# Performance work log

Hardware: AMD Instinct MI355X
Metric: run time of the kernel (lower is better)

Reference implementation:

```python
import jax, jax.numpy as jnp
import numpy as np

N, E, F, NC, G = 50000, 400000, 128, 10, 64
EPS_BN = 1e-5
NEG_SLOPE = 0.2


def gat_conv(x, src, dst, W, a_src, a_dst, b, H, C):
    # PyG GATConv (concat=True): h = xW reshaped [N,H,C]; edge score =
    # leaky_relu(a_src.h_j + a_dst.h_i); softmax over incoming edges of i;
    # out_i = sum_j alpha_ij * h_j, then bias.
    n = x.shape[0]
    h = (x @ W).reshape(n, H, C)
    s_src = jnp.sum(h * a_src, axis=-1)  # [N,H]
    s_dst = jnp.sum(h * a_dst, axis=-1)  # [N,H]
    e = jax.nn.leaky_relu(s_src[src] + s_dst[dst], NEG_SLOPE)  # [E',H]
    m = jax.ops.segment_max(e, dst, num_segments=n)
    e = jnp.exp(e - m[dst])
    z = jax.ops.segment_sum(e, dst, num_segments=n)
    alpha = e / (z[dst] + 1e-16)
    msg = h[src] * alpha[:, :, None]  # [E',H,C]
    out = jax.ops.segment_sum(msg, dst, num_segments=n)
    return out.reshape(n, H * C) + b


def batch_norm(x, g, b):
    mu = jnp.mean(x, axis=0)
    var = jnp.var(x, axis=0)
    return g * (x - mu) * jax.lax.rsqrt(var + EPS_BN) + b


def setup_inputs() -> dict:
    key = jax.random.key(0)
    ks = jax.random.split(key, 32)
    d = {}
    d["x"] = jax.random.normal(ks[0], (N, F), dtype=jnp.float32)
    d["edge_index"] = jax.random.randint(ks[1], (2, E), 0, N, dtype=jnp.int32)
    d["batch"] = jnp.sort(jax.random.randint(ks[2], (N,), 0, G, dtype=jnp.int32))

    def nrm(k, shape, scale=0.1):
        return jax.random.normal(k, shape, dtype=jnp.float32) * scale

    # GATConv1: F -> 16, heads=20
    d["W1"] = nrm(ks[3], (F, 20 * 16))
    d["as1"] = nrm(ks[4], (20, 16))
    d["ad1"] = nrm(ks[5], (20, 16))
    d["b1"] = jnp.zeros((320,), jnp.float32)
    d["g1"], d["be1"] = jnp.ones((320,), jnp.float32), jnp.zeros((320,), jnp.float32)
    d["lw1"], d["lb1"] = nrm(ks[6], (320, 16)), jnp.zeros((16,), jnp.float32)
    d["gl1"], d["bel1"] = jnp.ones((16,), jnp.float32), jnp.zeros((16,), jnp.float32)
    # GATConv2: 16 -> 32, heads=16
    d["W2"] = nrm(ks[7], (16, 16 * 32))
    d["as2"] = nrm(ks[8], (16, 32))
    d["ad2"] = nrm(ks[9], (16, 32))
    d["b2"] = jnp.zeros((512,), jnp.float32)
    d["g2"], d["be2"] = jnp.ones((512,), jnp.float32), jnp.zeros((512,), jnp.float32)
    d["lw2"], d["lb2"] = nrm(ks[10], (512, 32)), jnp.zeros((32,), jnp.float32)
    d["gl2"], d["bel2"] = jnp.ones((32,), jnp.float32), jnp.zeros((32,), jnp.float32)
    # GATConv3: 32 -> 48, heads=8
    d["W3"] = nrm(ks[11], (32, 8 * 48))
    d["as3"] = nrm(ks[12], (8, 48))
    d["ad3"] = nrm(ks[13], (8, 48))
    d["b3"] = jnp.zeros((384,), jnp.float32)
    d["g3"], d["be3"] = jnp.ones((384,), jnp.float32), jnp.zeros((384,), jnp.float32)
    d["lwf"], d["lbf"] = nrm(ks[14], (384, NC)), jnp.zeros((NC,), jnp.float32)
    return d


def reference(x, edge_index, batch, W1, as1, ad1, b1, g1, be1, lw1, lb1, gl1, bel1,
              W2, as2, ad2, b2, g2, be2, lw2, lb2, gl2, bel2,
              W3, as3, ad3, b3, g3, be3, lwf, lbf):
    n = x.shape[0]
    loops = jnp.arange(n, dtype=edge_index.dtype)
    src = jnp.concatenate([edge_index[0], loops])
    dst = jnp.concatenate([edge_index[1], loops])

    h = gat_conv(x, src, dst, W1, as1, ad1, b1, 20, 16)
    h = jax.nn.relu(batch_norm(h, g1, be1))
    h = h @ lw1 + lb1
    h = jax.nn.relu(batch_norm(h, gl1, bel1))

    h = gat_conv(h, src, dst, W2, as2, ad2, b2, 16, 32)
    h = jax.nn.relu(batch_norm(h, g2, be2))
    h = h @ lw2 + lb2
    h = jax.nn.relu(batch_norm(h, gl2, bel2))

    h = gat_conv(h, src, dst, W3, as3, ad3, b3, 8, 48)
    h = jax.nn.relu(batch_norm(h, g3, be3))

    # global_mean_pool over graph ids
    sums = jax.ops.segment_sum(h, batch, num_segments=G)
    cnts = jax.ops.segment_sum(jnp.ones((n,), h.dtype), batch, num_segments=G)
    pooled = sums / jnp.maximum(cnts, 1.0)[:, None]
    # dropout is identity in eval mode
    return pooled @ lwf + lbf
```

## Files before the change

### kernel.cpp

```cpp
#include <hip/hip_runtime.h>
#include <cstdint>
#include <cstddef>

#define N_NODES 50000
#define N_EDGES 400000
#define TOT_E   450000
#define G_GRAPHS 64
#define PB 2048
#define SCAN_B 98
#define GDB 1563

typedef unsigned short u16;
typedef unsigned int u32;
typedef unsigned char u8;
typedef __attribute__((ext_vector_type(8))) short s16x8;
typedef __attribute__((ext_vector_type(4))) float f32x4;
typedef __attribute__((ext_vector_type(2))) float f32x2;

__device__ __forceinline__ float b2f(u16 v) {
    union { u32 u; float f; } x; x.u = ((u32)v) << 16; return x.f;
}
__device__ __forceinline__ float lo2f(u32 u) {
    union { u32 u; float f; } x; x.u = u << 16; return x.f;
}
__device__ __forceinline__ float hi2f(u32 u) {
    union { u32 u; float f; } x; x.u = u & 0xffff0000u; return x.f;
}
__device__ __forceinline__ u16 f2b(float f) {
    union { float f; u32 u; } x; x.f = f;
    u32 r = x.u + 0x7fffu + ((x.u >> 16) & 1u);
    return (u16)(r >> 16);
}
__device__ __forceinline__ u32 pack2(float a, float b) {
    return (u32)f2b(a) | ((u32)f2b(b) << 16);
}

__global__ void k_init_deg(int* __restrict__ deg) {
    int i = blockIdx.x * blockDim.x + threadIdx.x;
    if (i < N_NODES) deg[i] = 1;
}

__global__ void k_hist(const int* __restrict__ ei, int* __restrict__ deg) {
    int e = blockIdx.x * blockDim.x + threadIdx.x;
    if (e < N_EDGES) atomicAdd(&deg[ei[N_EDGES + e]], 1);
}

__global__ void k_scan1(const int* __restrict__ deg, int* __restrict__ rowptr,
                        int* __restrict__ bsum) {
    __shared__ int buf[512];
    int tid = threadIdx.x;
    int i = blockIdx.x * 512 + tid;
    int v = (i < N_NODES) ? deg[i] : 0;
    buf[tid] = v;
    __syncthreads();
    for (int off = 1; off < 512; off <<= 1) {
        int t = (tid >= off) ? buf[tid - off] : 0;
        __syncthreads();
        buf[tid] += t;
        __syncthreads();
    }
    if (i < N_NODES) rowptr[i] = buf[tid] - v;
    if (tid == 511) bsum[blockIdx.x] = buf[511];
}

__global__ void k_scan2(int* __restrict__ bsum) {
    __shared__ int buf[128];
    int tid = threadIdx.x;
    int v = (tid < SCAN_B) ? bsum[tid] : 0;
    buf[tid] = v;
    __syncthreads();
    for (int off = 1; off < 128; off <<= 1) {
        int t = (tid >= off) ? buf[tid - off] : 0;
        __syncthreads();
        buf[tid] += t;
        __syncthreads();
    }
    if (tid < SCAN_B) bsum[tid] = buf[tid] - v;
}

__global__ void k_scan3(int* __restrict__ rowptr, int* __restrict__ cursor,
                        const int* __restrict__ bsum) {
    int i = blockIdx.x * blockDim.x + threadIdx.x;
    if (i < N_NODES) {
        int v = rowptr[i] + bsum[i >> 9];
        rowptr[i] = v;
        cursor[i] = v;
    }
    if (i == 0) rowptr[N_NODES] = TOT_E;
}

__global__ void k_scatter(const int* __restrict__ ei, int* __restrict__ cursor,
                          int* __restrict__ col, int* __restrict__ cdst) {
    int e = blockIdx.x * blockDim.x + threadIdx.x;
    if (e < N_EDGES) {
        int s = ei[e], d = ei[N_EDGES + e];
        int p = atomicAdd(&cursor[d], 1);
        col[p] = s;
        cdst[p] = d;
    } else if (e < TOT_E) {
        int i = e - N_EDGES;
        int p = atomicAdd(&cursor[i], 1);
        col[p] = i;
        cdst[p] = i;
    }
}

template<int K, int NO>
__global__ void k_wpack(const float* __restrict__ W, u16* __restrict__ Bp) {
    constexpr int KC = (K + 31) / 32;
    constexpr int NT = NO / 16;
    int idx = blockIdx.x * 256 + threadIdx.x;
    if (idx >= KC * NT * 64) return;
    int lane = idx & 63;
    int t = (idx >> 6) % NT;
    int c = (idx >> 6) / NT;
    int n = t * 16 + (lane & 15);
    int kbase = c * 32 + (lane >> 4) * 8;
    u16 v[8];
#pragma unroll
    for (int j = 0; j < 8; j++) {
        int k = kbase + j;
        v[j] = (k < K) ? f2b(W[(size_t)k * NO + n]) : (u16)0;
    }
    *(uint4*)(Bp + (size_t)idx * 8) = *(const uint4*)v;
}

template<int K, int NO, int H, int C>
__global__ void k_wtilde(const float* __restrict__ W, const float* __restrict__ as,
                         const float* __restrict__ ad, float* __restrict__ wts,
                         float* __restrict__ wtd) {
    static_assert((C % 4) == 0, "C divisible by 4");
    int t = threadIdx.x;
    if (t >= K * H) return;
    int k = t / H, h = t - k * H;
    float s1a = 0.f, s1b = 0.f, s1c = 0.f, s1d = 0.f;
    float s2a = 0.f, s2b = 0.f, s2c = 0.f, s2d = 0.f;
    const float* wr = W + (size_t)k * NO + h * C;
    const float* ar = as + h * C;
    const float* dr = ad + h * C;
    for (int c = 0; c < C; c += 4) {
        float w0 = wr[c], w1 = wr[c + 1], w2 = wr[c + 2], w3 = wr[c + 3];
        s1a = fmaf(w0, ar[c], s1a);     s1b = fmaf(w1, ar[c + 1], s1b);
        s1c = fmaf(w2, ar[c + 2], s1c); s1d = fmaf(w3, ar[c + 3], s1d);
        s2a = fmaf(w0, dr[c], s2a);     s2b = fmaf(w1, dr[c + 1], s2b);
        s2c = fmaf(w2, dr[c + 2], s2c); s2d = fmaf(w3, dr[c + 3], s2d);
    }
    wts[h * K + k] = (s1a + s1b) + (s1c + s1d);
    wtd[h * K + k] = (s2a + s2b) + (s2c + s2d);
}

template<int K>
__global__ void k_xform(const u16* __restrict__ X, const float* __restrict__ sc,
                        const float* __restrict__ sh, u16* __restrict__ Xt) {
    constexpr int NO2 = K / 2;
    int t = blockIdx.x * blockDim.x + threadIdx.x;
    if (t >= N_NODES * NO2) return;
    int w = t % NO2;
    u32 u = ((const u32*)X)[t];
    float2 scv = *(const float2*)&sc[2 * w];
    float2 shv = *(const float2*)&sh[2 * w];
    float a = fmaxf(lo2f(u) * scv.x + shv.x, 0.f);
    float b = fmaxf(hi2f(u) * scv.y + shv.y, 0.f);
    ((u32*)Xt)[t] = pack2(a, b);
}

template<int K, int H>
__global__ void k_scores_x(const u16* __restrict__ Xt, const float* __restrict__ wts,
                           const float* __restrict__ wtd, float* __restrict__ ssrc,
                           float* __restrict__ sdst) {
    int t = blockIdx.x * blockDim.x + threadIdx.x;
    if (t >= N_NODES * H) return;
    int i = t / H, h = t - i * H;
    const uint4* r = (const uint4*)(Xt + (size_t)i * K);
    const float4* ws = (const float4*)(wts + h * K);
    const float4* wd = (const float4*)(wtd + h * K);
    float s1 = 0.f, s2 = 0.f;
#pragma unroll
    for (int c8 = 0; c8 < K / 8; c8++) {
        uint4 u = r[c8];
        float v0 = lo2f(u.x), v1 = hi2f(u.x), v2 = lo2f(u.y), v3 = hi2f(u.y);
        float v4 = lo2f(u.z), v5 = hi2f(u.z), v6 = lo2f(u.w), v7 = hi2f(u.w);
        float4 aa = ws[c8 * 2], ab = ws[c8 * 2 + 1];
        float4 da = wd[c8 * 2], db = wd[c8 * 2 + 1];
        s1 = fmaf(v0, aa.x, fmaf(v1, aa.y, fmaf(v2, aa.z, fmaf(v3, aa.w, s1))));
        s1 = fmaf(v4, ab.x, fmaf(v5, ab.y, fmaf(v6, ab.z, fmaf(v7, ab.w, s1))));
        s2 = fmaf(v0, da.x, fmaf(v1, da.y, fmaf(v2, da.z, fmaf(v3, da.w, s2))));
        s2 = fmaf(v4, db.x, fmaf(v5, db.y, fmaf(v6, db.z, fmaf(v7, db.w, s2))));
    }
    ssrc[t] = s1;
    sdst[t] = s2;
}

template<int H, int K>
__global__ void k_aggx(const u16* __restrict__ Xt, const float* __restrict__ ssrc,
                       const float* __restrict__ sdst, const int* __restrict__ rowptr,
                       const int* __restrict__ col, u16* __restrict__ M) {
    constexpr int WPR = K / 2;
    constexpr int EPR = 64 / WPR;
    constexpr int Q = K / 4;
    static_assert(H * K == 256, "m row must be 256 elems (4/lane)");
    int wid = (int)((blockIdx.x * blockDim.x + threadIdx.x) >> 6);
    int lane = threadIdx.x & 63;
    if (wid >= N_NODES) return;
    int hl = lane / Q;
    int q = lane % Q;
    int lslot = lane / WPR;
    int lword = lane % WPR;
    float sd = (lane < H) ? sdst[(size_t)wid * H + lane] : 0.f;
    f32x2 acc01 = {0.f, 0.f}, acc23 = {0.f, 0.f};
    float z = 0.f;
    int beg = rowptr[wid], end = rowptr[wid + 1];
    for (int base = beg; base < end; base += 64) {
        int nmax = min(64, end - base);
        int myc = (base + lane < end) ? col[base + lane] : 0;
        int j = 0;
        for (; j + EPR <= nmax; j += EPR) {
            int ce = __shfl(myc, j + lslot);
            u32 g = *(const u32*)(Xt + (size_t)ce * K + lword * 2);
            int se[EPR];
#pragma unroll
            for (int e = 0; e < EPR; e++) se[e] = __shfl(myc, j + e);
            float w[EPR];
#pragma unroll
            for (int e = 0; e < EPR; e++) w[e] = 0.f;
            if (lane < H) {
#pragma unroll
                for (int e = 0; e < EPR; e++) {
                    float v = ssrc[(size_t)se[e] * H + lane] + sd;
                    v = (v > 0.f) ? v : 0.2f * v;
                    w[e] = __expf(v);
                    z += w[e];
                }
            }
#pragma unroll
            for (int e = 0; e < EPR; e++) {
                float al = __shfl(w[e], hl);
                u32 xa = __shfl(g, e * WPR + 2 * q);
                u32 xb = __shfl(g, e * WPR + 2 * q + 1);
                f32x2 al2 = {al, al};
                f32x2 xa2 = {lo2f(xa), hi2f(xa)};
                f32x2 xb2 = {lo2f(xb), hi2f(xb)};
                acc01 += xa2 * al2;
                acc23 += xb2 * al2;
            }
        }
        for (; j < nmax; j++) {
            int se = __shfl(myc, j);
            u32 g = *(const u32*)(Xt + (size_t)se * K + lword * 2);
            float w0 = 0.f;
            if (lane < H) {
                float v = ssrc[(size_t)se * H + lane] + sd;
                v = (v > 0.f) ? v : 0.2f * v;
                w0 = __expf(v);
                z += w0;
            }
            float al = __shfl(w0, hl);
            u32 xa = __shfl(g, 2 * q);
            u32 xb = __shfl(g, 2 * q + 1);
            f32x2 al2 = {al, al};
            f32x2 xa2 = {lo2f(xa), hi2f(xa)};
            f32x2 xb2 = {lo2f(xb), hi2f(xb)};
            acc01 += xa2 * al2;
            acc23 += xb2 * al2;
        }
    }
    float zk = __shfl(z, hl);
    float inv = 1.0f / (zk + 1e-16f);
    uint2 o;
    o.x = pack2(acc01.x * inv, acc01.y * inv);
    o.y = pack2(acc23.x * inv, acc23.y * inv);
    u32* orow = (u32*)(M + (size_t)wid * (H * K));
    *(uint2*)&orow[hl * WPR + 2 * q] = o;
}

template<int K, int NO, int C>
__global__ void k_gemmd(const u16* __restrict__ M, const u16* __restrict__ Bp,
                        const float* __restrict__ wb, u16* __restrict__ Y,
                        float* __restrict__ pbuf) {
    constexpr int NT = NO / 16;
    constexpr int TS = NT / 2;
    constexpr int HK = (NO / C) * K;
    __shared__ float ls[2 * NO];
    int tid = threadIdx.x;
    for (int i = tid; i < 2 * NO; i += 256) ls[i] = 0.f;
    __syncthreads();
    int lane = tid & 63;
    int wv = __builtin_amdgcn_readfirstlane(tid >> 6);
    int sid = blockIdx.x * 4 + wv;
    int rt = sid >> 1, ch = sid & 1;
    int rbase = rt * 16;
    int m = lane & 15, quad = lane >> 4;
    bool tileok = rbase < N_NODES;
    int arow = rbase + m;
    if (arow >= N_NODES) arow = N_NODES - 1;
    const u16* xr = M + (size_t)arow * HK;
    if (tileok) {
        for (int tt = 0; tt < TS; tt++) {
            int t = ch * TS + tt;
            int h = (t * 16) / C;
            s16x8 a;
            if (K == 32 || quad < 2) {
                a = *(const s16x8*)(xr + h * K + quad * 8);
            } else {
#pragma unroll
                for (int j = 0; j < 8; j++) a[j] = 0;
            }
            s16x8 b = *(const s16x8*)(Bp + ((size_t)(t * 64 + lane)) * 8);
            f32x4 z4 = (f32x4){0.f, 0.f, 0.f, 0.f};
            f32x4 acc = __builtin_amdgcn_mfma_f32_16x16x32_bf16(a, b, z4, 0, 0, 0);
            int colb = t * 16 + m;
            float bv = wb[colb];
            float s = 0.f, q = 0.f;
#pragma unroll
            for (int i = 0; i < 4; i++) {
                int grow = rbase + quad * 4 + i;
                float v = acc[i] + bv;
                Y[(size_t)grow * NO + colb] = f2b(v);
                s += v;
                q += v * v;
            }
            s += __shfl_xor(s, 16); s += __shfl_xor(s, 32);
            q += __shfl_xor(q, 16); q += __shfl_xor(q, 32);
            if (quad == 0) {
                atomicAdd(&ls[colb], s);
                atomicAdd(&ls[NO + colb], q);
            }
        }
    }
    __syncthreads();
    float* dst = pbuf + (size_t)blockIdx.x * (2 * NO);
    for (int i = tid; i < 2 * NO; i += 256) dst[i] = ls[i];
}

__global__ void k_bnfinalg(const float* __restrict__ pbuf, const float* __restrict__ g,
                           const float* __restrict__ be, float* __restrict__ scale,
                           float* __restrict__ shift, int NO, int NB) {
    __shared__ float s1[256], s2[256];
    int col = blockIdx.x;
    int tid = threadIdx.x;
    float a = 0.f, b = 0.f;
    for (int bk = tid; bk < NB; bk += 256) {
        a += pbuf[(size_t)bk * 2 * NO + col];
        b += pbuf[(size_t)bk * 2 * NO + NO + col];
    }
    s1[tid] = a;
    s2[tid] = b;
    __syncthreads();
    for (int off = 128; off > 0; off >>= 1) {
        if (tid < off) {
            s1[tid] += s1[tid + off];
            s2[tid] += s2[tid + off];
        }
        __syncthreads();
    }
    if (tid == 0) {
        float mu = s1[0] / (float)N_NODES;
        float var = s2[0] / (float)N_NODES - mu * mu;
        float sc = g[col] * rsqrtf(var + 1e-5f);
        scale[col] = sc;
        shift[col] = be[col] - mu * sc;
    }
}

template<int K, int NO, bool XFORM>
__global__ __launch_bounds__(256, 2)
void k_gemm(const float* __restrict__ X, const u16* __restrict__ Bp,
            const float* __restrict__ scale, const float* __restrict__ shift,
            u16* __restrict__ Y) {
    constexpr int KC = (K + 31) / 32;
    constexpr int NT = NO / 16;
    int lane = threadIdx.x & 63;
    int wv = __builtin_amdgcn_readfirstlane((int)(threadIdx.x >> 6));
    int rbase = blockIdx.x * 64 + wv * 16;
    int m = lane & 15, quad = lane >> 4;
    int arow = rbase + m;
    if (arow >= N_NODES) arow = N_NODES - 1;
    const float* xr = X + (size_t)arow * K;

    f32x4 acc[NT];
#pragma unroll
    for (int t = 0; t < NT; t++) acc[t] = (f32x4){0.f, 0.f, 0.f, 0.f};

    for (int c = 0; c < KC; c++) {
        int kbase = c * 32 + quad * 8;
        float xv[8];
        if (kbase < K) {
            float4 va = *(const float4*)&xr[kbase];
            float4 vb = *(const float4*)&xr[kbase + 4];
            xv[0] = va.x; xv[1] = va.y; xv[2] = va.z; xv[3] = va.w;
            xv[4] = vb.x; xv[5] = vb.y; xv[6] = vb.z; xv[7] = vb.w;
            if (XFORM) {
                float4 sa = *(const float4*)&scale[kbase];
                float4 sb = *(const float4*)&scale[kbase + 4];
                float4 ha = *(const float4*)&shift[kbase];
                float4 hb = *(const float4*)&shift[kbase + 4];
                xv[0] = fmaxf(xv[0] * sa.x + ha.x, 0.f);
                xv[1] = fmaxf(xv[1] * sa.y + ha.y, 0.f);
                xv[2] = fmaxf(xv[2] * sa.z + ha.z, 0.f);
                xv[3] = fmaxf(xv[3] * sa.w + ha.w, 0.f);
                xv[4] = fmaxf(xv[4] * sb.x + hb.x, 0.f);
                xv[5] = fmaxf(xv[5] * sb.y + hb.y, 0.f);
                xv[6] = fmaxf(xv[6] * sb.z + hb.z, 0.f);
                xv[7] = fmaxf(xv[7] * sb.w + hb.w, 0.f);
            }
        } else {
#pragma unroll
            for (int j = 0; j < 8; j++) xv[j] = 0.f;
        }
        s16x8 a;
#pragma unroll
        for (int j = 0; j < 8; j++) a[j] = (short)f2b(xv[j]);

        const u16* bp = Bp + (size_t)(c * NT) * 64 * 8;
#pragma unroll
        for (int t = 0; t < NT; t++) {
            s16x8 b = *(const s16x8*)(bp + ((size_t)(t * 64 + lane)) * 8);
            acc[t] = __builtin_amdgcn_mfma_f32_16x16x32_bf16(a, b, acc[t], 0, 0, 0);
        }
    }

#pragma unroll
    for (int t = 0; t < NT; t++) {
        int colb = t * 16 + m;
#pragma unroll
        for (int i = 0; i < 4; i++) {
            int grow = rbase + quad * 4 + i;
            if (grow < N_NODES) Y[(size_t)grow * NO + colb] = f2b(acc[t][i]);
        }
    }
}

template<int K, int NO, bool XFORM, bool BIAS>
__global__ __launch_bounds__(256, 2)
void k_gemmb(const u16* __restrict__ X, const u16* __restrict__ Bp,
             const float* __restrict__ scale, const float* __restrict__ shift,
             const float* __restrict__ wb, u16* __restrict__ Y) {
    constexpr int KC = (K + 31) / 32;
    constexpr int NT = NO / 16;
    int lane = threadIdx.x & 63;
    int wv = __builtin_amdgcn_readfirstlane((int)(threadIdx.x >> 6));
    int rbase = blockIdx.x * 64 + wv * 16;
    int m = lane & 15, quad = lane >> 4;
    int arow = rbase + m;
    if (arow >= N_NODES) arow = N_NODES - 1;
    const u32* xr = (const u32*)(X + (size_t)arow * K);

    f32x4 acc[NT];
#pragma unroll
    for (int t = 0; t < NT; t++) acc[t] = (f32x4){0.f, 0.f, 0.f, 0.f};

    for (int c = 0; c < KC; c++) {
        int kbase = c * 32 + quad * 8;
        s16x8 a;
        if (kbase < K) {
            uint4 w = *(const uint4*)&xr[kbase >> 1];
            if (XFORM) {
                float xv[8];
                xv[0] = lo2f(w.x); xv[1] = hi2f(w.x);
                xv[2] = lo2f(w.y); xv[3] = hi2f(w.y);
                xv[4] = lo2f(w.z); xv[5] = hi2f(w.z);
                xv[6] = lo2f(w.w); xv[7] = hi2f(w.w);
                float4 sa = *(const float4*)&scale[kbase];
                float4 sb = *(const float4*)&scale[kbase + 4];
                float4 ha = *(const float4*)&shift[kbase];
                float4 hb = *(const float4*)&shift[kbase + 4];
                xv[0] = fmaxf(xv[0] * sa.x + ha.x, 0.f);
                xv[1] = fmaxf(xv[1] * sa.y + ha.y, 0.f);
                xv[2] = fmaxf(xv[2] * sa.z + ha.z, 0.f);
                xv[3] = fmaxf(xv[3] * sa.w + ha.w, 0.f);
                xv[4] = fmaxf(xv[4] * sb.x + hb.x, 0.f);
                xv[5] = fmaxf(xv[5] * sb.y + hb.y, 0.f);
                xv[6] = fmaxf(xv[6] * sb.z + hb.z, 0.f);
                xv[7] = fmaxf(xv[7] * sb.w + hb.w, 0.f);
#pragma unroll
                for (int j = 0; j < 8; j++) a[j] = (short)f2b(xv[j]);
            } else {
                a = *(const s16x8*)&w;
            }
        } else {
#pragma unroll
            for (int j = 0; j < 8; j++) a[j] = 0;
        }

        const u16* bp = Bp + (size_t)(c * NT) * 64 * 8;
#pragma unroll
        for (int t = 0; t < NT; t++) {
            s16x8 b = *(const s16x8*)(bp + ((size_t)(t * 64 + lane)) * 8);
            acc[t] = __builtin_amdgcn_mfma_f32_16x16x32_bf16(a, b, acc[t], 0, 0, 0);
        }
    }

#pragma unroll
    for (int t = 0; t < NT; t++) {
        int colb = t * 16 + m;
        float bv = BIAS ? wb[colb] : 0.f;
#pragma unroll
        for (int i = 0; i < 4; i++) {
            int grow = rbase + quad * 4 + i;
            if (grow < N_NODES) Y[(size_t)grow * NO + colb] = f2b(acc[t][i] + bv);
        }
    }
}

template<int H, int C>
__global__ void k_scores(const u16* __restrict__ Hm, const float* __restrict__ asrc,
                         const float* __restrict__ adst, float* __restrict__ ssrc,
                         float* __restrict__ sdst, u8* __restrict__ H8) {
    static_assert(C == 16, "fp8 emit assumes C==16");
    int t = blockIdx.x * blockDim.x + threadIdx.x;
    if (t >= N_NODES * H) return;
    int i = t / H, h = t - i * H;
    const uint4* row4 = (const uint4*)(Hm + (size_t)i * H * C + h * C);
    const float4* a4 = (const float4*)(asrc + h * C);
    const float4* d4 = (const float4*)(adst + h * C);
    float s1 = 0.f, s2 = 0.f;
    uint4 q8;
    u32* qw = (u32*)&q8;
#pragma unroll
    for (int c8 = 0; c8 < C / 8; c8++) {
        uint4 u = row4[c8];
        float v0 = lo2f(u.x), v1 = hi2f(u.x), v2 = lo2f(u.y), v3 = hi2f(u.y);
        float v4 = lo2f(u.z), v5 = hi2f(u.z), v6 = lo2f(u.w), v7 = hi2f(u.w);
        float4 aa = a4[c8 * 2], ab = a4[c8 * 2 + 1];
        float4 da = d4[c8 * 2], db = d4[c8 * 2 + 1];
        s1 = fmaf(v0, aa.x, fmaf(v1, aa.y, fmaf(v2, aa.z, fmaf(v3, aa.w, s1))));
        s1 = fmaf(v4, ab.x, fmaf(v5, ab.y, fmaf(v6, ab.z, fmaf(v7, ab.w, s1))));
        s2 = fmaf(v0, da.x, fmaf(v1, da.y, fmaf(v2, da.z, fmaf(v3, da.w, s2))));
        s2 = fmaf(v4, db.x, fmaf(v5, db.y, fmaf(v6, db.z, fmaf(v7, db.w, s2))));
        u32 qa = 0, qb = 0;
        qa = __builtin_amdgcn_cvt_pk_fp8_f32(v0, v1, qa, false);
        qa = __builtin_amdgcn_cvt_pk_fp8_f32(v2, v3, qa, true);
        qb = __builtin_amdgcn_cvt_pk_fp8_f32(v4, v5, qb, false);
        qb = __builtin_amdgcn_cvt_pk_fp8_f32(v6, v7, qb, true);
        qw[c8 * 2] = qa;
        qw[c8 * 2 + 1] = qb;
    }
    ssrc[t] = s1;
    sdst[t] = s2;
    *(uint4*)(H8 + (size_t)i * (H * C) + h * C) = q8;
}

template<int H, int C>
__global__ void k_agg8(const u8* __restrict__ Hm8, const float* __restrict__ ssrc,
                       const float* __restrict__ sdst, const int* __restrict__ rowptr,
                       const int* __restrict__ col, const float* __restrict__ bias,
                       u16* __restrict__ out) {
    constexpr int HC = H * C;
    constexpr int W2 = HC / 8;
    static_assert(W2 <= 64, "row must fit 64 uint2");
    static_assert((C % 8) == 0, "8-col block must stay within one head");
    int wid = (int)((blockIdx.x * blockDim.x + threadIdx.x) >> 6);
    int lane = threadIdx.x & 63;
    if (wid >= N_NODES) return;
    int hl = (8 * lane) / C;
    int gidx = (lane < W2) ? lane : 0;
    float sd = (lane < H) ? sdst[(size_t)wid * H + lane] : 0.f;
    f32x2 acc01 = {0.f, 0.f}, acc23 = {0.f, 0.f};
    f32x2 acc45 = {0.f, 0.f}, acc67 = {0.f, 0.f};
    float z = 0.f;
    int beg = rowptr[wid], end = rowptr[wid + 1];
#define ACC8(gg, wk) { \
        f32x2 wv_ = {wk, wk}; \
        acc01 += __builtin_amdgcn_cvt_pk_f32_fp8(gg.x, false) * wv_; \
        acc23 += __builtin_amdgcn_cvt_pk_f32_fp8(gg.x, true) * wv_; \
        acc45 += __builtin_amdgcn_cvt_pk_f32_fp8(gg.y, false) * wv_; \
        acc67 += __builtin_amdgcn_cvt_pk_f32_fp8(gg.y, true) * wv_; }
    for (int base = beg; base < end; base += 64) {
        int nmax = min(64, end - base);
        int myc = (base + lane < end) ? col[base + lane] : 0;
        int j = 0;
        for (; j + 4 <= nmax; j += 4) {
            int s0 = __shfl(myc, j), s1 = __shfl(myc, j + 1);
            int s2 = __shfl(myc, j + 2), s3 = __shfl(myc, j + 3);
            uint2 g0 = ((const uint2*)(Hm8 + (size_t)s0 * HC))[gidx];
            uint2 g1 = ((const uint2*)(Hm8 + (size_t)s1 * HC))[gidx];
            uint2 g2 = ((const uint2*)(Hm8 + (size_t)s2 * HC))[gidx];
            uint2 g3 = ((const uint2*)(Hm8 + (size_t)s3 * HC))[gidx];
            float w0 = 0.f, w1 = 0.f, w2 = 0.f, w3 = 0.f;
            if (lane < H) {
                float v0 = ssrc[(size_t)s0 * H + lane] + sd;
                float v1 = ssrc[(size_t)s1 * H + lane] + sd;
                float v2 = ssrc[(size_t)s2 * H + lane] + sd;
                float v3 = ssrc[(size_t)s3 * H + lane] + sd;
                v0 = (v0 > 0.f) ? v0 : 0.2f * v0;
                v1 = (v1 > 0.f) ? v1 : 0.2f * v1;
                v2 = (v2 > 0.f) ? v2 : 0.2f * v2;
                v3 = (v3 > 0.f) ? v3 : 0.2f * v3;
                w0 = __expf(v0); w1 = __expf(v1);
                w2 = __expf(v2); w3 = __expf(v3);
                z += (w0 + w1) + (w2 + w3);
            }
            float wk0 = __shfl(w0, hl), wk1 = __shfl(w1, hl);
            float wk2 = __shfl(w2, hl), wk3 = __shfl(w3, hl);
            ACC8(g0, wk0)
            ACC8(g1, wk1)
            ACC8(g2, wk2)
            ACC8(g3, wk3)
        }
        for (; j < nmax; j++) {
            int s0 = __shfl(myc, j);
            uint2 g0 = ((const uint2*)(Hm8 + (size_t)s0 * HC))[gidx];
            float w0 = 0.f;
            if (lane < H) {
                float v = ssrc[(size_t)s0 * H + lane] + sd;
                v = (v > 0.f) ? v : 0.2f * v;
                w0 = __expf(v);
                z += w0;
            }
            float wk0 = __shfl(w0, hl);
            ACC8(g0, wk0)
        }
    }
#undef ACC8
    float zk = __shfl(z, hl);
    if (lane < W2) {
        float inv = 1.0f / (zk + 1e-16f);
        const float4* b4 = (const float4*)(bias + 8 * lane);
        float4 ba = b4[0], bb = b4[1];
        uint4 o;
        o.x = pack2(fmaf(acc01.x, inv, ba.x), fmaf(acc01.y, inv, ba.y));
        o.y = pack2(fmaf(acc23.x, inv, ba.z), fmaf(acc23.y, inv, ba.w));
        o.z = pack2(fmaf(acc45.x, inv, bb.x), fmaf(acc45.y, inv, bb.y));
        o.w = pack2(fmaf(acc67.x, inv, bb.z), fmaf(acc67.y, inv, bb.w));
        ((uint4*)(out + (size_t)wid * HC))[lane] = o;
    }
}

template<int NO>
__global__ void k_bnstats(const u16* __restrict__ X, float* __restrict__ psum,
                          float* __restrict__ psumsq) {
    constexpr int NO2 = NO / 2;
    constexpr int RPS = (NO2 >= 256) ? 1 : ((255 + NO2) / NO2);
    constexpr int BS = NO2 * RPS;
    __shared__ float2 ls[BS], ls2[BS];
    int c2 = threadIdx.x % NO2;
    int rsub = threadIdx.x / NO2;
    constexpr int chunk = (N_NODES + PB - 1) / PB;
    int r0 = blockIdx.x * chunk;
    int r1 = min(N_NODES, r0 + chunk);
    float2 s = make_float2(0.f, 0.f), s2 = make_float2(0.f, 0.f);
    const u32* Xw = (const u32*)X;
#pragma unroll 4
    for (int r = r0 + rsub; r < r1; r += RPS) {
        u32 u = Xw[(size_t)r * NO2 + c2];
        float a = lo2f(u), b = hi2f(u);
        s.x += a; s.y += b;
        s2.x += a * a; s2.y += b * b;
    }
    if (RPS > 1) {
        ls[threadIdx.x] = s;
        ls2[threadIdx.x] = s2;
        __syncthreads();
        for (int off = BS / 2; off >= NO2; off >>= 1) {
            if (threadIdx.x < off) {
                ls[threadIdx.x].x += ls[threadIdx.x + off].x;
                ls[threadIdx.x].y += ls[threadIdx.x + off].y;
                ls2[threadIdx.x].x += ls2[threadIdx.x + off].x;
                ls2[threadIdx.x].y += ls2[threadIdx.x + off].y;
            }
            __syncthreads();
        }
        s = ls[threadIdx.x];
        s2 = ls2[threadIdx.x];
    }
    if (rsub == 0) {
        *(float2*)&psum[(size_t)blockIdx.x * NO + 2 * c2] = s;
        *(float2*)&psumsq[(size_t)blockIdx.x * NO + 2 * c2] = s2;
    }
}

__global__ void k_bnfinal(const float* __restrict__ psum, const float* __restrict__ psumsq,
                          const float* __restrict__ g, const float* __restrict__ be,
                          float* __restrict__ scale, float* __restrict__ shift, int NO) {
    __shared__ float s1[256], s2[256];
    int col = blockIdx.x;
    int tid = threadIdx.x;
    float a = 0.f, b = 0.f;
    for (int bk = tid; bk < PB; bk += 256) {
        a += psum[(size_t)bk * NO + col];
        b += psumsq[(size_t)bk * NO + col];
    }
    s1[tid] = a;
    s2[tid] = b;
    __syncthreads();
    for (int off = 128; off > 0; off >>= 1) {
        if (tid < off) {
            s1[tid] += s1[tid + off];
            s2[tid] += s2[tid + off];
        }
        __syncthreads();
    }
    if (tid == 0) {
        float mu = s1[0] / (float)N_NODES;
        float var = s2[0] / (float)N_NODES - mu * mu;
        float sc = g[col] * rsqrtf(var + 1e-5f);
        scale[col] = sc;
        shift[col] = be[col] - mu * sc;
    }
}

__global__ void k_bhist(const int* __restrict__ batch, int* __restrict__ cnt) {
    __shared__ int h[G_GRAPHS];
    int tid = threadIdx.x;
    if (tid < G_GRAPHS) h[tid] = 0;
    __syncthreads();
    int i = blockIdx.x * blockDim.x + tid;
    if (i < N_NODES) atomicAdd(&h[batch[i]], 1);
    __syncthreads();
    if (tid < G_GRAPHS) atomicAdd(&cnt[tid], h[tid]);
}

__global__ void k_pool(const u16* __restrict__ X, const int* __restrict__ batch,
                       const float* __restrict__ sc, const float* __restrict__ sh,
                       float* __restrict__ pooled) {
    int t2 = threadIdx.x;
    const int chunk = (N_NODES + gridDim.x - 1) / gridDim.x;
    int r0 = blockIdx.x * chunk;
    int r1 = min(N_NODES, r0 + chunk);
    if (r0 >= N_NODES) return;
    float2 scv = *(const float2*)&sc[2 * t2];
    float2 shv = *(const float2*)&sh[2 * t2];
    const u32* Xw = (const u32*)X;
    float2 acc = make_float2(0.f, 0.f);
    int cur = batch[r0];
    for (int r = r0; r < r1; r++) {
        int gid = batch[r];
        if (gid != cur) {
            atomicAdd(&pooled[(size_t)cur * 384 + 2 * t2], acc.x);
            atomicAdd(&pooled[(size_t)cur * 384 + 2 * t2 + 1], acc.y);
            acc = make_float2(0.f, 0.f);
            cur = gid;
        }
        u32 u = Xw[(size_t)r * 192 + t2];
        acc.x += fmaxf(lo2f(u) * scv.x + shv.x, 0.f);
        acc.y += fmaxf(hi2f(u) * scv.y + shv.y, 0.f);
    }
    atomicAdd(&pooled[(size_t)cur * 384 + 2 * t2], acc.x);
    atomicAdd(&pooled[(size_t)cur * 384 + 2 * t2 + 1], acc.y);
}

__global__ void k_final(const float* __restrict__ pooled, const int* __restrict__ cnt,
                        const float* __restrict__ lwf, const float* __restrict__ lbf,
                        float* __restrict__ out) {
    int wid = (int)((blockIdx.x * blockDim.x + threadIdx.x) >> 6);
    int lane = threadIdx.x & 63;
    if (wid >= G_GRAPHS * 10) return;
    int g = wid / 10, c = wid - g * 10;
    float inv = 1.0f / fmaxf((float)cnt[g], 1.0f);
    float acc = 0.f;
    for (int k = lane; k < 384; k += 64)
        acc += pooled[(size_t)g * 384 + k] * lwf[k * 10 + c];
#pragma unroll
    for (int off = 32; off > 0; off >>= 1) acc += __shfl_xor(acc, off);
    if (lane == 0) out[wid] = acc * inv + lbf[c];
}

extern "C" void kernel_launch(void* const* d_in, const int* in_sizes, int n_in,
                              void* d_out, int out_size, void* d_ws, size_t ws_size,
                              hipStream_t stream) {
    const float* x    = (const float*)d_in[0];
    const int*   ei   = (const int*)d_in[1];
    const int*   batch= (const int*)d_in[2];
    const float* W1   = (const float*)d_in[3];
    const float* as1  = (const float*)d_in[4];
    const float* ad1  = (const float*)d_in[5];
    const float* b1   = (const float*)d_in[6];
    const float* g1   = (const float*)d_in[7];
    const float* be1  = (const float*)d_in[8];
    const float* lw1  = (const float*)d_in[9];
    const float* lb1  = (const float*)d_in[10];
    const float* gl1  = (const float*)d_in[11];
    const float* bel1 = (const float*)d_in[12];
    const float* W2   = (const float*)d_in[13];
    const float* as2  = (const float*)d_in[14];
    const float* ad2  = (const float*)d_in[15];
    const float* b2   = (const float*)d_in[16];
    const float* g2   = (const float*)d_in[17];
    const float* be2  = (const float*)d_in[18];
    const float* lw2  = (const float*)d_in[19];
    const float* lb2  = (const float*)d_in[20];
    const float* gl2  = (const float*)d_in[21];
    const float* bel2 = (const float*)d_in[22];
    const float* W3   = (const float*)d_in[23];
    const float* as3  = (const float*)d_in[24];
    const float* ad3  = (const float*)d_in[25];
    const float* b3   = (const float*)d_in[26];
    const float* g3   = (const float*)d_in[27];
    const float* be3  = (const float*)d_in[28];
    const float* lwf  = (const float*)d_in[29];
    const float* lbf  = (const float*)d_in[30];
    float* out = (float*)d_out;

    char* p = (char*)d_ws;
    auto alloc = [&](size_t bytes) {
        char* r = p;
        p += (bytes + 255) & ~(size_t)255;
        return r;
    };
    int*   rowptr = (int*)alloc(4 * (size_t)(N_NODES + 1));
    int*   cursor = (int*)alloc(4 * (size_t)N_NODES);
    int*   deg    = (int*)alloc(4 * (size_t)N_NODES);
    int*   bsum   = (int*)alloc(4 * (size_t)(SCAN_B + 1));
    int*   col    = (int*)alloc(4 * (size_t)TOT_E);
    int*   cdst   = (int*)alloc(4 * (size_t)TOT_E);
    float* ssrc   = (float*)alloc(4 * (size_t)N_NODES * 20);
    float* sdst   = (float*)alloc(4 * (size_t)N_NODES * 20);
    u16*   hbuf   = (u16*)alloc(2 * (size_t)N_NODES * 512);
    u16*   obuf   = (u16*)alloc(2 * (size_t)N_NODES * 512);
    u16*   xbuf   = (u16*)alloc(2 * (size_t)N_NODES * 32);
    u16*   xtil   = (u16*)alloc(2 * (size_t)N_NODES * 32);
    u8*    hbuf8  = (u8*)alloc((size_t)N_NODES * 320);
    float* psum   = (float*)alloc(4 * (size_t)PB * 512);
    float* psumsq = (float*)alloc(4 * (size_t)PB * 512);
    float* gpart  = (float*)alloc(4 * (size_t)GDB * 1024);
    float* scA    = (float*)alloc(4 * 512);
    float* shA    = (float*)alloc(4 * 512);
    float* scB    = (float*)alloc(4 * 64);
    float* shB    = (float*)alloc(4 * 64);
    float* wts    = (float*)alloc(4 * 256);
    float* wtd    = (float*)alloc(4 * 256);
    float* pooled = (float*)alloc(4 * (size_t)G_GRAPHS * 384);
    int*   cnt    = (int*)alloc(4 * G_GRAPHS);
    u16*   bp1    = (u16*)alloc(2 * (size_t)4 * 20 * 64 * 8);
    u16*   bp2    = (u16*)alloc(2 * (size_t)1 * 32 * 64 * 8);
    u16*   bp3    = (u16*)alloc(2 * (size_t)1 * 24 * 64 * 8);
    u16*   bpl1   = (u16*)alloc(2 * (size_t)10 * 1 * 64 * 8);
    u16*   bpl2   = (u16*)alloc(2 * (size_t)16 * 2 * 64 * 8);
    u16*   mbuf   = hbuf;

    const int LB = (N_NODES + 63) / 64;

    k_init_deg<<<(N_NODES + 255) / 256, 256, 0, stream>>>(deg);
    k_hist<<<(N_EDGES + 255) / 256, 256, 0, stream>>>(ei, deg);
    k_scan1<<<SCAN_B, 512, 0, stream>>>(deg, rowptr, bsum);
    k_scan2<<<1, 128, 0, stream>>>(bsum);
    k_scan3<<<(N_NODES + 255) / 256, 256, 0, stream>>>(rowptr, cursor, bsum);
    k_scatter<<<(TOT_E + 255) / 256, 256, 0, stream>>>(ei, cursor, col, cdst);
    k_wpack<128, 320><<<20, 256, 0, stream>>>(W1, bp1);
    k_wpack<16, 512><<<8, 256, 0, stream>>>(W2, bp2);
    k_wpack<32, 384><<<6, 256, 0, stream>>>(W3, bp3);
    k_wpack<320, 16><<<3, 256, 0, stream>>>(lw1, bpl1);
    k_wpack<512, 32><<<8, 256, 0, stream>>>(lw2, bpl2);
    hipMemsetAsync(pooled, 0, 4 * (size_t)G_GRAPHS * 384 + 256, stream);

    k_gemm<128, 320, false><<<LB, 256, 0, stream>>>(x, bp1, nullptr, nullptr, hbuf);
    k_scores<20, 16><<<(N_NODES * 20 + 255) / 256, 256, 0, stream>>>(hbuf, as1, ad1, ssrc, sdst, hbuf8);
    k_agg8<20, 16><<<(N_NODES + 3) / 4, 256, 0, stream>>>(hbuf8, ssrc, sdst, rowptr, col, b1, obuf);
    k_bnstats<320><<<PB, 320, 0, stream>>>(obuf, psum, psumsq);
    k_bnfinal<<<320, 256, 0, stream>>>(psum, psumsq, g1, be1, scA, shA, 320);
    k_gemmb<320, 16, true, true><<<LB, 256, 0, stream>>>(obuf, bpl1, scA, shA, lb1, xbuf);
    k_bnstats<16><<<PB, 256, 0, stream>>>(xbuf, psum, psumsq);
    k_bnfinal<<<16, 256, 0, stream>>>(psum, psumsq, gl1, bel1, scB, shB, 16);

    k_wtilde<16, 512, 16, 32><<<1, 256, 0, stream>>>(W2, as2, ad2, wts, wtd);
    k_xform<16><<<(N_NODES * 8 + 255) / 256, 256, 0, stream>>>(xbuf, scB, shB, xtil);
    k_scores_x<16, 16><<<(N_NODES * 16 + 255) / 256, 256, 0, stream>>>(xtil, wts, wtd, ssrc, sdst);
    k_aggx<16, 16><<<(N_NODES + 3) / 4, 256, 0, stream>>>(xtil, ssrc, sdst, rowptr, col, mbuf);
    k_gemmd<16, 512, 32><<<GDB, 256, 0, stream>>>(mbuf, bp2, b2, obuf, gpart);
    k_bnfinalg<<<512, 256, 0, stream>>>(gpart, g2, be2, scA, shA, 512, GDB);
    k_gemmb<512, 32, true, true><<<LB, 256, 0, stream>>>(obuf, bpl2, scA, shA, lb2, xbuf);
    k_bnstats<32><<<PB, 256, 0, stream>>>(xbuf, psum, psumsq);
    k_bnfinal<<<32, 256, 0, stream>>>(psum, psumsq, gl2, bel2, scB, shB, 32);

    k_wtilde<32, 384, 8, 48><<<1, 256, 0, stream>>>(W3, as3, ad3, wts, wtd);
    k_xform<32><<<(N_NODES * 16 + 255) / 256, 256, 0, stream>>>(xbuf, scB, shB, xtil);
    k_scores_x<32, 8><<<(N_NODES * 8 + 255) / 256, 256, 0, stream>>>(xtil, wts, wtd, ssrc, sdst);
    k_aggx<8, 32><<<(N_NODES + 3) / 4, 256, 0, stream>>>(xtil, ssrc, sdst, rowptr, col, mbuf);
    k_gemmd<32, 384, 48><<<GDB, 256, 0, stream>>>(mbuf, bp3, b3, obuf, gpart);
    k_bnfinalg<<<384, 256, 0, stream>>>(gpart, g3, be3, scA, shA, 384, GDB);

    k_bhist<<<(N_NODES + 255) / 256, 256, 0, stream>>>(batch, cnt);
    k_pool<<<2048, 192, 0, stream>>>(obuf, batch, scA, shA, pooled);
    k_final<<<160, 256, 0, stream>>>(pooled, cnt, lwf, lbf, out);
}
```

Before: 528.8 us.

## Emit fp8 directly from layer-1 GEMM and compute scores from x via folded weights

The first GAT layer's GEMM now writes fp8 features directly, using swapped MFMA operands so each lane holds four consecutive columns for a packed 32-bit store. The bf16 intermediate buffer and the separate scores pass that reread it are dropped. Attention scores are instead computed straight from x with precomputed W·a_src and W·a_dst vectors, using a wave-per-node reduction. This removes a 50000x320 bf16 write and read, at the cost of rereading x and a small extra weight-folding kernel. Scores now come from fp32 x rather than bf16-rounded h, which slightly changes numerics.

```diff
diff --git a/kernel.cpp b/kernel.cpp
--- a/kernel.cpp
+++ b/kernel.cpp
@@ -147,6 +147,59 @@
     }
     wts[h * K + k] = (s1a + s1b) + (s1c + s1d);
     wtd[h * K + k] = (s2a + s2b) + (s2c + s2d);
+}
+
+template<int K, int NO, int H, int C>
+__global__ void k_wtilde1(const float* __restrict__ W, const float* __restrict__ as,
+                          const float* __restrict__ ad, float* __restrict__ wts,
+                          float* __restrict__ wtd) {
+    int t = blockIdx.x * blockDim.x + threadIdx.x;
+    if (t >= K * H) return;
+    int k = t / H, h = t - k * H;
+    float s1 = 0.f, s2 = 0.f;
+    const float* wr = W + (size_t)k * NO + h * C;
+    const float* ar = as + h * C;
+    const float* dr = ad + h * C;
+    for (int c = 0; c < C; c++) {
+        float wv = wr[c];
+        s1 = fmaf(wv, ar[c], s1);
+        s2 = fmaf(wv, dr[c], s2);
+    }
+    wts[k * H + h] = s1;
+    wtd[k * H + h] = s2;
+}
+
+template<int K, int H>
+__global__ void k_scores1(const float* __restrict__ X, const float* __restrict__ wts,
+                          const float* __restrict__ wtd, float* __restrict__ ssrc,
+                          float* __restrict__ sdst) {
+    static_assert(K == 128 && H == 20, "layout assumes K=128,H=20");
+    int wid = (int)((blockIdx.x * blockDim.x + threadIdx.x) >> 6);
+    int lane = threadIdx.x & 63;
+    if (wid >= N_NODES) return;
+    int g = lane >> 4, l = lane & 15;
+    const float* xr = X + (size_t)wid * K + l * 8;
+    float4 xa = *(const float4*)xr;
+    float4 xb = *(const float4*)(xr + 4);
+    float xv[8] = {xa.x, xa.y, xa.z, xa.w, xb.x, xb.y, xb.z, xb.w};
+#pragma unroll
+    for (int hh = 0; hh < 5; hh++) {
+        int h = g * 5 + hh;
+        float p1 = 0.f, p2 = 0.f;
+#pragma unroll
+        for (int j = 0; j < 8; j++) {
+            p1 = fmaf(xv[j], wts[(l * 8 + j) * H + h], p1);
+            p2 = fmaf(xv[j], wtd[(l * 8 + j) * H + h], p2);
+        }
+        p1 += __shfl_xor(p1, 1); p1 += __shfl_xor(p1, 2);
+        p1 += __shfl_xor(p1, 4); p1 += __shfl_xor(p1, 8);
+        p2 += __shfl_xor(p2, 1); p2 += __shfl_xor(p2, 2);
+        p2 += __shfl_xor(p2, 4); p2 += __shfl_xor(p2, 8);
+        if (l == 0) {
+            ssrc[(size_t)wid * H + h] = p1;
+            sdst[(size_t)wid * H + h] = p2;
+        }
+    }
 }
 
 template<int K>
@@ -362,11 +415,10 @@
     }
 }
 
-template<int K, int NO, bool XFORM>
+template<int K, int NO>
 __global__ __launch_bounds__(256, 2)
-void k_gemm(const float* __restrict__ X, const u16* __restrict__ Bp,
-            const float* __restrict__ scale, const float* __restrict__ shift,
-            u16* __restrict__ Y) {
+void k_gemm8(const float* __restrict__ X, const u16* __restrict__ Bp,
+             u8* __restrict__ H8) {
     constexpr int KC = (K + 31) / 32;
     constexpr int NT = NO / 16;
     int lane = threadIdx.x & 63;
@@ -374,7 +426,8 @@
     int rbase = blockIdx.x * 64 + wv * 16;
     int m = lane & 15, quad = lane >> 4;
     int arow = rbase + m;
-    if (arow >= N_NODES) arow = N_NODES - 1;
+    bool rowok = arow < N_NODES;
+    if (!rowok) arow = N_NODES - 1;
     const float* xr = X + (size_t)arow * K;
 
     f32x4 acc[NT];
@@ -383,49 +436,30 @@
 
     for (int c = 0; c < KC; c++) {
         int kbase = c * 32 + quad * 8;
-        float xv[8];
-        if (kbase < K) {
-            float4 va = *(const float4*)&xr[kbase];
-            float4 vb = *(const float4*)&xr[kbase + 4];
-            xv[0] = va.x; xv[1] = va.y; xv[2] = va.z; xv[3] = va.w;
-            xv[4] = vb.x; xv[5] = vb.y; xv[6] = vb.z; xv[7] = vb.w;
-            if (XFORM) {
-                float4 sa = *(const float4*)&scale[kbase];
-                float4 sb = *(const float4*)&scale[kbase + 4];
-                float4 ha = *(const float4*)&shift[kbase];
-                float4 hb = *(const float4*)&shift[kbase + 4];
-                xv[0] = fmaxf(xv[0] * sa.x + ha.x, 0.f);
-                xv[1] = fmaxf(xv[1] * sa.y + ha.y, 0.f);
-                xv[2] = fmaxf(xv[2] * sa.z + ha.z, 0.f);
-                xv[3] = fmaxf(xv[3] * sa.w + ha.w, 0.f);
-                xv[4] = fmaxf(xv[4] * sb.x + hb.x, 0.f);
-                xv[5] = fmaxf(xv[5] * sb.y + hb.y, 0.f);
-                xv[6] = fmaxf(xv[6] * sb.z + hb.z, 0.f);
-                xv[7] = fmaxf(xv[7] * sb.w + hb.w, 0.f);
-            }
-        } else {
-#pragma unroll
-            for (int j = 0; j < 8; j++) xv[j] = 0.f;
-        }
+        float4 va = *(const float4*)&xr[kbase];
+        float4 vb = *(const float4*)&xr[kbase + 4];
         s16x8 a;
-#pragma unroll
-        for (int j = 0; j < 8; j++) a[j] = (short)f2b(xv[j]);
+        a[0] = (short)f2b(va.x); a[1] = (short)f2b(va.y);
+        a[2] = (short)f2b(va.z); a[3] = (short)f2b(va.w);
+        a[4] = (short)f2b(vb.x); a[5] = (short)f2b(vb.y);
+        a[6] = (short)f2b(vb.z); a[7] = (short)f2b(vb.w);
 
         const u16* bp = Bp + (size_t)(c * NT) * 64 * 8;
 #pragma unroll
         for (int t = 0; t < NT; t++) {
             s16x8 b = *(const s16x8*)(bp + ((size_t)(t * 64 + lane)) * 8);
-            acc[t] = __builtin_amdgcn_mfma_f32_16x16x32_bf16(a, b, acc[t], 0, 0, 0);
+            acc[t] = __builtin_amdgcn_mfma_f32_16x16x32_bf16(b, a, acc[t], 0, 0, 0);
         }
     }
 
 #pragma unroll
     for (int t = 0; t < NT; t++) {
-        int colb = t * 16 + m;
-#pragma unroll
-        for (int i = 0; i < 4; i++) {
-            int grow = rbase + quad * 4 + i;
-            if (grow < N_NODES) Y[(size_t)grow * NO + colb] = f2b(acc[t][i]);
+        int colb = t * 16 + quad * 4;
+        if (rowok) {
+            u32 q = 0;
+            q = __builtin_amdgcn_cvt_pk_fp8_f32(acc[t][0], acc[t][1], q, false);
+            q = __builtin_amdgcn_cvt_pk_fp8_f32(acc[t][2], acc[t][3], q, true);
+            *(u32*)(H8 + (size_t)arow * NO + colb) = q;
         }
     }
 }
@@ -500,44 +534,6 @@
             if (grow < N_NODES) Y[(size_t)grow * NO + colb] = f2b(acc[t][i] + bv);
         }
     }
-}
-
-template<int H, int C>
-__global__ void k_scores(const u16* __restrict__ Hm, const float* __restrict__ asrc,
-                         const float* __restrict__ adst, float* __restrict__ ssrc,
-                         float* __restrict__ sdst, u8* __restrict__ H8) {
-    static_assert(C == 16, "fp8 emit assumes C==16");
-    int t = blockIdx.x * blockDim.x + threadIdx.x;
-    if (t >= N_NODES * H) return;
-    int i = t / H, h = t - i * H;
-    const uint4* row4 = (const uint4*)(Hm + (size_t)i * H * C + h * C);
-    const float4* a4 = (const float4*)(asrc + h * C);
-    const float4* d4 = (const float4*)(adst + h * C);
-    float s1 = 0.f, s2 = 0.f;
-    uint4 q8;
-    u32* qw = (u32*)&q8;
-#pragma unroll
-    for (int c8 = 0; c8 < C / 8; c8++) {
-        uint4 u = row4[c8];
-        float v0 = lo2f(u.x), v1 = hi2f(u.x), v2 = lo2f(u.y), v3 = hi2f(u.y);
-        float v4 = lo2f(u.z), v5 = hi2f(u.z), v6 = lo2f(u.w), v7 = hi2f(u.w);
-        float4 aa = a4[c8 * 2], ab = a4[c8 * 2 + 1];
-        float4 da = d4[c8 * 2], db = d4[c8 * 2 + 1];
-        s1 = fmaf(v0, aa.x, fmaf(v1, aa.y, fmaf(v2, aa.z, fmaf(v3, aa.w, s1))));
-        s1 = fmaf(v4, ab.x, fmaf(v5, ab.y, fmaf(v6, ab.z, fmaf(v7, ab.w, s1))));
-        s2 = fmaf(v0, da.x, fmaf(v1, da.y, fmaf(v2, da.z, fmaf(v3, da.w, s2))));
-        s2 = fmaf(v4, db.x, fmaf(v5, db.y, fmaf(v6, db.z, fmaf(v7, db.w, s2))));
-        u32 qa = 0, qb = 0;
-        qa = __builtin_amdgcn_cvt_pk_fp8_f32(v0, v1, qa, false);
-        qa = __builtin_amdgcn_cvt_pk_fp8_f32(v2, v3, qa, true);
-        qb = __builtin_amdgcn_cvt_pk_fp8_f32(v4, v5, qb, false);
-        qb = __builtin_amdgcn_cvt_pk_fp8_f32(v6, v7, qb, true);
-        qw[c8 * 2] = qa;
-        qw[c8 * 2 + 1] = qb;
-    }
-    ssrc[t] = s1;
-    sdst[t] = s2;
-    *(uint4*)(H8 + (size_t)i * (H * C) + h * C) = q8;
 }
 
 template<int H, int C>
@@ -819,6 +815,8 @@
     float* shB    = (float*)alloc(4 * 64);
     float* wts    = (float*)alloc(4 * 256);
     float* wtd    = (float*)alloc(4 * 256);
+    float* wts1   = (float*)alloc(4 * 2560);
+    float* wtd1   = (float*)alloc(4 * 2560);
     float* pooled = (float*)alloc(4 * (size_t)G_GRAPHS * 384);
     int*   cnt    = (int*)alloc(4 * G_GRAPHS);
     u16*   bp1    = (u16*)alloc(2 * (size_t)4 * 20 * 64 * 8);
@@ -841,10 +839,11 @@
     k_wpack<32, 384><<<6, 256, 0, stream>>>(W3, bp3);
     k_wpack<320, 16><<<3, 256, 0, stream>>>(lw1, bpl1);
     k_wpack<512, 32><<<8, 256, 0, stream>>>(lw2, bpl2);
+    k_wtilde1<128, 320, 20, 16><<<10, 256, 0, stream>>>(W1, as1, ad1, wts1, wtd1);
     hipMemsetAsync(pooled, 0, 4 * (size_t)G_GRAPHS * 384 + 256, stream);
 
-    k_gemm<128, 320, false><<<LB, 256, 0, stream>>>(x, bp1, nullptr, nullptr, hbuf);
-    k_scores<20, 16><<<(N_NODES * 20 + 255) / 256, 256, 0, stream>>>(hbuf, as1, ad1, ssrc, sdst, hbuf8);
+    k_gemm8<128, 320><<<LB, 256, 0, stream>>>(x, bp1, hbuf8);
+    k_scores1<128, 20><<<(N_NODES + 3) / 4, 256, 0, stream>>>(x, wts1, wtd1, ssrc, sdst);
     k_agg8<20, 16><<<(N_NODES + 3) / 4, 256, 0, stream>>>(hbuf8, ssrc, sdst, rowptr, col, b1, obuf);
     k_bnstats<320><<<PB, 320, 0, stream>>>(obuf, psum, psumsq);
     k_bnfinal<<<320, 256, 0, stream>>>(psum, psumsq, g1, be1, scA, shA, 320);
```

Result: slower. 954.1 us (+80.4%).
